# Kernel tuning notes

Hardware: AMD Instinct MI355X
Metric: run time of the kernel (lower is better)

Reference implementation:

```python
import jax, jax.numpy as jnp
import numpy as np

B, S, D = 2, 2048, 1024
H = 16
HD = D // H  # 64
SCALE = 1.0 / np.sqrt(HD).astype(np.float32)


def setup_inputs() -> dict:
    key = jax.random.key(0)
    ks = jax.random.split(key, 5)
    std = 0.02
    return {
        "x": jax.random.normal(ks[0], (B, S, D), dtype=jnp.float32),
        "W_qkv": jax.random.normal(ks[1], (D, 3 * D), dtype=jnp.float32) * std,
        "b_qkv": jnp.zeros((3 * D,), dtype=jnp.float32),
        "W_proj": jax.random.normal(ks[2], (D, D), dtype=jnp.float32) * std,
        "b_proj": jnp.zeros((D,), dtype=jnp.float32),
    }


def reference(x, W_qkv, b_qkv, W_proj, b_proj):
    bsz, seq_len, _ = x.shape
    qkv = x @ W_qkv + b_qkv  # [B,S,3D]
    qkv = qkv.reshape(bsz, seq_len, 3, H, HD)
    qkv = jnp.transpose(qkv, (2, 0, 3, 1, 4))  # [3,B,H,S,HD]
    q, k, v = qkv[0], qkv[1], qkv[2]
    scores = jnp.einsum("bhqd,bhkd->bhqk", q, k) * SCALE  # [B,H,S,S]
    causal = jnp.tril(jnp.ones((seq_len, seq_len), dtype=bool))
    scores = jnp.where(causal[None, None], scores, -jnp.inf)
    weights = jax.nn.softmax(scores, axis=-1)
    attn = jnp.einsum("bhqk,bhkd->bhqd", weights, v)  # [B,H,S,HD]
    attn = jnp.transpose(attn, (0, 2, 1, 3)).reshape(bsz, seq_len, H * HD)
    return attn @ W_proj + b_proj
```

## Files before the change

### kernel.cpp

```cpp
#include <hip/hip_runtime.h>
#include <stdint.h>

#define NB 2
#define NS 2048
#define ND 1024
#define NH 16
#define NHD 64
#define SCALE_QL2 0.1803368801111244f

typedef __attribute__((ext_vector_type(8))) short bf16x8;
typedef __attribute__((ext_vector_type(4))) float f32x4;
typedef __attribute__((ext_vector_type(16))) float f32x16;

__device__ __forceinline__ unsigned short f2bf(float f) {
  union { float f; unsigned u; } v; v.f = f;
  unsigned r = v.u + 0x7FFFu + ((v.u >> 16) & 1u);
  return (unsigned short)(r >> 16);
}

__device__ __forceinline__ float fexp2(float x) { return __builtin_amdgcn_exp2f(x); }

__device__ __forceinline__ unsigned cvtpk(float a, float b) {
  unsigned r;
  asm("v_cvt_pk_bf16_f32 %0, %1, %2" : "=v"(r) : "v"(a), "v"(b));
  return r;
}

__device__ __forceinline__ void plswap(unsigned& a, unsigned& b) {
  asm("v_permlane32_swap_b32 %0, %1" : "+v"(a), "+v"(b));
}

__device__ __forceinline__ void gload16(const void* g, void* l) {
  __builtin_amdgcn_global_load_lds(
      (const __attribute__((address_space(1))) unsigned int*)g,
      (__attribute__((address_space(3))) unsigned int*)l, 16, 0, 0);
}


__global__ void cvt_x(const float* __restrict__ in, unsigned short* __restrict__ out) {
  int i = blockIdx.x * 256 + threadIdx.x;
  const float4* p = (const float4*)in + (size_t)i * 2;
  float4 a = p[0], b = p[1];
  typedef __attribute__((ext_vector_type(8))) unsigned short u16x8;
  u16x8 o;
  o[0] = f2bf(a.x); o[1] = f2bf(a.y); o[2] = f2bf(a.z); o[3] = f2bf(a.w);
  o[4] = f2bf(b.x); o[5] = f2bf(b.y); o[6] = f2bf(b.z); o[7] = f2bf(b.w);
  *((u16x8*)out + i) = o;
}

__global__ void transpose_cvt(const float* __restrict__ W, unsigned short* __restrict__ WT,
                              int rows, int cols) {
  __shared__ float tile[32][33];
  int bc = blockIdx.x * 32;
  int br = blockIdx.y * 32;
  int tx = threadIdx.x & 31, ty = threadIdx.x >> 5;
#pragma unroll
  for (int i = 0; i < 4; ++i)
    tile[ty + i * 8][tx] = W[(size_t)(br + ty + i * 8) * cols + bc + tx];
  __syncthreads();
#pragma unroll
  for (int i = 0; i < 4; ++i)
    WT[(size_t)(bc + ty + i * 8) * rows + br + tx] = f2bf(tile[tx][ty + i * 8]);
}

template <int EPI>
__global__ __launch_bounds__(256, 2) void gemm_bt(
    const unsigned short* __restrict__ A, const unsigned short* __restrict__ Bt,
    const float* __restrict__ bias, int NT,
    unsigned short* __restrict__ Oq, unsigned short* __restrict__ Ok,
    unsigned short* __restrict__ Ov, float* __restrict__ Of) {
  __shared__ __align__(16) unsigned short lA[128 * 64];
  __shared__ __align__(16) unsigned short lB[128 * 64];

  int bid = blockIdx.x;
  int cpx = gridDim.x >> 3;
  int swz = (bid & 7) * cpx + (bid >> 3);
  int mt = swz / NT, nt = swz % NT;
  int m0 = mt * 128, n0 = nt * 128;

  int t = threadIdx.x, lane = t & 63, w = t >> 6;
  int wm = w >> 1, wn = w & 1;

  f32x4 acc[4][4] = {};

  const char* gA = (const char*)(A + (size_t)m0 * 1024);
  const char* gB = (const char*)(Bt + (size_t)n0 * 1024);

  for (int kt = 0; kt < 16; ++kt) {
    __syncthreads();
#pragma unroll
    for (int r = 0; r < 4; ++r) {
      int L = r * 4096 + w * 1024 + lane * 16;
      int row = L >> 7, cb = L & 127;
      int scb = cb ^ ((row & 7) << 4);
      gload16(gA + (size_t)row * 2048 + kt * 128 + scb, (char*)lA + (L - lane * 16));
      gload16(gB + (size_t)row * 2048 + kt * 128 + scb, (char*)lB + (L - lane * 16));
    }
    __syncthreads();
#pragma unroll
    for (int kk = 0; kk < 2; ++kk) {
      bf16x8 af[4], bg[4];
#pragma unroll
      for (int mi = 0; mi < 4; ++mi) {
        int row = wm * 64 + mi * 16 + (lane & 15);
        int byte = row * 128 + ((kk * 64 + (lane >> 4) * 16) ^ ((row & 7) << 4));
        af[mi] = *(const bf16x8*)((const char*)lA + byte);
      }
#pragma unroll
      for (int ni = 0; ni < 4; ++ni) {
        int row = wn * 64 + ni * 16 + (lane & 15);
        int byte = row * 128 + ((kk * 64 + (lane >> 4) * 16) ^ ((row & 7) << 4));
        bg[ni] = *(const bf16x8*)((const char*)lB + byte);
      }
#pragma unroll
      for (int mi = 0; mi < 4; ++mi)
#pragma unroll
        for (int ni = 0; ni < 4; ++ni)
          acc[mi][ni] = __builtin_amdgcn_mfma_f32_16x16x32_bf16(af[mi], bg[ni], acc[mi][ni], 0, 0, 0);
    }
  }

#pragma unroll
  for (int mi = 0; mi < 4; ++mi)
#pragma unroll
    for (int ni = 0; ni < 4; ++ni) {
      int col = n0 + wn * 64 + ni * 16 + (lane & 15);
      float bv = bias[col];
#pragma unroll
      for (int r = 0; r < 4; ++r) {
        int row = m0 + wm * 64 + mi * 16 + (lane >> 4) * 4 + r;
        float v = acc[mi][ni][r] + bv;
        if (EPI == 0) {
          int which = col >> 10, dd = col & 1023;
          int h = dd >> 6, hd = dd & 63;
          int b = row >> 11, s = row & 2047;
          size_t bh = (size_t)(b * 16 + h);
          if (which == 0)      Oq[(bh * 2048 + s) * 64 + hd] = f2bf(v * SCALE_QL2);
          else if (which == 1) Ok[(bh * 2048 + s) * 64 + hd] = f2bf(v);
          else                 Ov[(bh * 64 + hd) * 2048 + s] = f2bf(v);
        } else {
          Of[(size_t)row * 1024 + col] = v;
        }
      }
    }
}

__global__ __launch_bounds__(128, 2) void attn_fwd(
    const unsigned short* __restrict__ Qb, const unsigned short* __restrict__ Kb,
    const unsigned short* __restrict__ Vt, unsigned short* __restrict__ Ao) {
  __shared__ __align__(16) unsigned short lK[2][64 * 64];
  __shared__ __align__(16) unsigned short lV[2][64 * 64];

  int id = blockIdx.x;
  int qt = 31 - (id >> 5);
  int bh = id & 31;
  int t = threadIdx.x, lane = t & 63, w = t >> 6;
  int lo = lane & 31, hi = lane >> 5;
  int q0w = qt * 64 + w * 32;
  int swz = (lo & 7) << 4;

  const unsigned short* Qg = Qb + ((size_t)bh * 2048 + q0w + lo) * 64 + hi * 8;
  bf16x8 qf[4];
#pragma unroll
  for (int kk = 0; kk < 4; ++kk) qf[kk] = *(const bf16x8*)(Qg + kk * 16);

  f32x16 o0 = {}, o1 = {};
  float m = -1e30f, lsum = 0.f;

  const char* Kg = (const char*)(Kb + (size_t)bh * 2048 * 64);
  const char* Vg = (const char*)(Vt + (size_t)bh * 64 * 2048);

  int Lb = w * 4096 + lane * 16;
  auto STAGE = [&](int buf, int tile) {
    int s0 = tile * 64;
#pragma unroll
    for (int r = 0; r < 4; ++r) {
      int L = r * 1024 + Lb;
      int row = L >> 7, cb = L & 127;
      int scb = cb ^ ((row & 7) << 4);
      gload16(Kg + (size_t)(s0 + row) * 128 + scb, (char*)&lK[buf][0] + (L - lane * 16));
      gload16(Vg + (size_t)row * 4096 + (size_t)s0 * 2 + scb, (char*)&lV[buf][0] + (L - lane * 16));
    }
  };

  int ntiles = qt + 1;
  STAGE(0, 0);

  int cur = 0;
  for (int it = 0; it < ntiles; ++it) {
    if (it + 1 < ntiles) {
      STAGE(cur ^ 1, it + 1);
      asm volatile("s_waitcnt vmcnt(8)" ::: "memory");
    } else {
      asm volatile("s_waitcnt vmcnt(0)" ::: "memory");
    }
    asm volatile("s_barrier" ::: "memory");

    const char* bK = (const char*)&lK[cur][0];
    const char* bV = (const char*)&lV[cur][0];

    f32x16 sv0 = {}, sv1 = {};
    __builtin_amdgcn_s_setprio(1);
#pragma unroll
    for (int kk = 0; kk < 4; ++kk) {
      int dby = 32 * kk + 16 * hi;
      bf16x8 k0 = *(const bf16x8*)(bK + lo * 128 + (dby ^ swz));
      bf16x8 k1 = *(const bf16x8*)(bK + (32 + lo) * 128 + (dby ^ swz));
      sv0 = __builtin_amdgcn_mfma_f32_32x32x16_bf16(k0, qf[kk], sv0, 0, 0, 0);
      sv1 = __builtin_amdgcn_mfma_f32_32x32x16_bf16(k1, qf[kk], sv1, 0, 0, 0);
    }
    __builtin_amdgcn_s_setprio(0);

    if (it == ntiles - 1) {
      int qg = q0w + lo, s0 = it * 64;
#pragma unroll
      for (int r = 0; r < 16; ++r) {
        int kv = s0 + (r & 3) + 8 * (r >> 2) + 4 * hi;
        if (kv > qg) sv0[r] = -1e30f;
        if (kv + 32 > qg) sv1[r] = -1e30f;
      }
    }

    float rmax = -1e30f;
#pragma unroll
    for (int r = 0; r < 16; ++r) rmax = fmaxf(rmax, fmaxf(sv0[r], sv1[r]));
    rmax = fmaxf(rmax, __shfl_xor(rmax, 32));

    if (__any(rmax > m + 8.0f)) {
      float mn = fmaxf(m, rmax);
      float sf = fexp2(m - mn);
      m = mn; lsum *= sf;
#pragma unroll
      for (int r = 0; r < 16; ++r) {
        float s = __shfl(sf, (r & 3) + 8 * (r >> 2) + 4 * hi);
        o0[r] *= s; o1[r] *= s;
      }
    }

    float rsum = 0.f;
#pragma unroll
    for (int r = 0; r < 16; ++r) {
      sv0[r] = fexp2(sv0[r] - m); rsum += sv0[r];
      sv1[r] = fexp2(sv1[r] - m); rsum += sv1[r];
    }
    rsum += __shfl_xor(rsum, 32);
    lsum += rsum;

    bf16x8 pa[4];
#pragma unroll
    for (int h2 = 0; h2 < 2; ++h2) {
      const f32x16& P = h2 ? sv1 : sv0;
#pragma unroll
      for (int kp = 0; kp < 2; ++kp) {
        unsigned a0 = cvtpk(P[8 * kp + 0], P[8 * kp + 1]);
        unsigned a1 = cvtpk(P[8 * kp + 2], P[8 * kp + 3]);
        unsigned b0 = cvtpk(P[8 * kp + 4], P[8 * kp + 5]);
        unsigned b1 = cvtpk(P[8 * kp + 6], P[8 * kp + 7]);
        plswap(a0, b0); plswap(a1, b1);
        union { unsigned u[4]; bf16x8 v; } uu;
        uu.u[0] = a0; uu.u[1] = a1; uu.u[2] = b0; uu.u[3] = b1;
        pa[2 * h2 + kp] = uu.v;
      }
    }

    __builtin_amdgcn_s_setprio(1);
#pragma unroll
    for (int dh = 0; dh < 2; ++dh) {
      f32x16& oc = dh ? o1 : o0;
#pragma unroll
      for (int ks = 0; ks < 4; ++ks) {
        int kvby = 32 * ks + 16 * hi;
        bf16x8 vf = *(const bf16x8*)(bV + (32 * dh + lo) * 128 + (kvby ^ swz));
        oc = __builtin_amdgcn_mfma_f32_32x32x16_bf16(pa[ks], vf, oc, 0, 0, 0);
      }
    }
    __builtin_amdgcn_s_setprio(0);

    asm volatile("s_barrier" ::: "memory");
    cur ^= 1;
  }

  float rl = 1.0f / lsum;
  int b = bh >> 4, hh = bh & 15;
#pragma unroll
  for (int r = 0; r < 16; ++r) {
    int qrow = (r & 3) + 8 * (r >> 2) + 4 * hi;
    float s = __shfl(rl, qrow);
    size_t base = ((size_t)(b * 2048 + q0w + qrow)) * 1024 + hh * 64 + lo;
    Ao[base]      = f2bf(o0[r] * s);
    Ao[base + 32] = f2bf(o1[r] * s);
  }
}

extern "C" void kernel_launch(void* const* d_in, const int* in_sizes, int n_in,
                              void* d_out, int out_size, void* d_ws, size_t ws_size,
                              hipStream_t stream) {
  const float* x      = (const float*)d_in[0];
  const float* W_qkv  = (const float*)d_in[1];
  const float* b_qkv  = (const float*)d_in[2];
  const float* W_proj = (const float*)d_in[3];
  const float* b_proj = (const float*)d_in[4];
  float* out = (float*)d_out;

  char* ws = (char*)d_ws;
  const size_t MB = 1u << 20;
  unsigned short* xb     = (unsigned short*)(ws);
  unsigned short* WqkvT  = (unsigned short*)(ws + 8 * MB);
  unsigned short* WprojT = (unsigned short*)(ws + 14 * MB);
  unsigned short* Qb     = (unsigned short*)(ws + 16 * MB);
  unsigned short* Kb     = (unsigned short*)(ws + 24 * MB);
  unsigned short* Vt     = (unsigned short*)(ws + 32 * MB);
  unsigned short* attn   = xb;

  cvt_x<<<2048, 256, 0, stream>>>(x, xb);
  transpose_cvt<<<dim3(96, 32), 256, 0, stream>>>(W_qkv, WqkvT, 1024, 3072);
  transpose_cvt<<<dim3(32, 32), 256, 0, stream>>>(W_proj, WprojT, 1024, 1024);
  gemm_bt<0><<<768, 256, 0, stream>>>(xb, WqkvT, b_qkv, 24, Qb, Kb, Vt, nullptr);
  attn_fwd<<<1024, 128, 0, stream>>>(Qb, Kb, Vt, attn);
  gemm_bt<1><<<256, 256, 0, stream>>>(attn, WprojT, b_proj, 8, nullptr, nullptr, nullptr, out);
}
```

Baseline: 129.4 us.

## Split causal attention over KV chunks with a separate combine kernel

Causal attention is split along the key/value axis: each query tile is divided into chunks of up to 8 KV tiles, giving 2560 blocks of roughly equal work instead of 1024 blocks whose work varies 1 to 32 tiles. Each split writes unnormalized bf16 partial outputs plus row max and sum, and a new combine kernel merges them with log-sum-exp weighting. This targets load imbalance and the long tail from the largest query tiles. In exchange it adds an extra launch, partial-output traffic to workspace and a bf16 rounding of the partials. The path only runs when the workspace is large enough, otherwise the original kernel is used.

```diff
diff --git a/kernel.cpp b/kernel.cpp
--- a/kernel.cpp
+++ b/kernel.cpp
@@ -11,6 +11,7 @@
 typedef __attribute__((ext_vector_type(8))) short bf16x8;
 typedef __attribute__((ext_vector_type(4))) float f32x4;
 typedef __attribute__((ext_vector_type(16))) float f32x16;
+typedef __attribute__((ext_vector_type(8))) unsigned short u16x8;
 
 __device__ __forceinline__ unsigned short f2bf(float f) {
   union { float f; unsigned u; } v; v.f = f;
@@ -18,6 +19,11 @@
   return (unsigned short)(r >> 16);
 }
 
+__device__ __forceinline__ float bf2f(unsigned short u) {
+  union { unsigned u; float f; } v; v.u = ((unsigned)u) << 16;
+  return v.f;
+}
+
 __device__ __forceinline__ float fexp2(float x) { return __builtin_amdgcn_exp2f(x); }
 
 __device__ __forceinline__ unsigned cvtpk(float a, float b) {
@@ -41,7 +47,6 @@
   int i = blockIdx.x * 256 + threadIdx.x;
   const float4* p = (const float4*)in + (size_t)i * 2;
   float4 a = p[0], b = p[1];
-  typedef __attribute__((ext_vector_type(8))) unsigned short u16x8;
   u16x8 o;
   o[0] = f2bf(a.x); o[1] = f2bf(a.y); o[2] = f2bf(a.z); o[3] = f2bf(a.w);
   o[4] = f2bf(b.x); o[5] = f2bf(b.y); o[6] = f2bf(b.z); o[7] = f2bf(b.w);
@@ -145,19 +150,31 @@
     }
 }
 
-__global__ __launch_bounds__(128, 2) void attn_fwd(
+__global__ __launch_bounds__(128, 2) void attn_split(
     const unsigned short* __restrict__ Qb, const unsigned short* __restrict__ Kb,
-    const unsigned short* __restrict__ Vt, unsigned short* __restrict__ Ao) {
+    const unsigned short* __restrict__ Vt,
+    unsigned short* __restrict__ PO, float* __restrict__ PML) {
   __shared__ __align__(16) unsigned short lK[2][64 * 64];
   __shared__ __align__(16) unsigned short lV[2][64 * 64];
 
   int id = blockIdx.x;
-  int qt = 31 - (id >> 5);
   int bh = id & 31;
+  int slot = id >> 5;
+  int a, g;
+  if (slot < 8)       { a = 0; g = slot; }
+  else if (slot < 24) { a = 1; g = slot - 8; }
+  else if (slot < 48) { a = 2; g = slot - 24; }
+  else                { a = 3; g = slot - 48; }
+  int qg = (a == 0) ? g : (a == 1) ? (g >> 1) : (a == 2) ? ((g * 11) >> 5) : (g >> 2);
+  int qt = a * 8 + qg;
+  int c  = g - qg * (a + 1);
+  int t0 = c * 8;
+  int tend = min(t0 + 7, qt);
+
   int t = threadIdx.x, lane = t & 63, w = t >> 6;
   int lo = lane & 31, hi = lane >> 5;
   int q0w = qt * 64 + w * 32;
-  int swz = (lo & 7) << 4;
+  int swzb = (lo & 7) << 4;
 
   const unsigned short* Qg = Qb + ((size_t)bh * 2048 + q0w + lo) * 64 + hi * 8;
   bf16x8 qf[4];
@@ -183,12 +200,11 @@
     }
   };
 
-  int ntiles = qt + 1;
-  STAGE(0, 0);
+  STAGE(0, t0);
 
   int cur = 0;
-  for (int it = 0; it < ntiles; ++it) {
-    if (it + 1 < ntiles) {
+  for (int it = t0; it <= tend; ++it) {
+    if (it < tend) {
       STAGE(cur ^ 1, it + 1);
       asm volatile("s_waitcnt vmcnt(8)" ::: "memory");
     } else {
@@ -204,20 +220,20 @@
 #pragma unroll
     for (int kk = 0; kk < 4; ++kk) {
       int dby = 32 * kk + 16 * hi;
-      bf16x8 k0 = *(const bf16x8*)(bK + lo * 128 + (dby ^ swz));
-      bf16x8 k1 = *(const bf16x8*)(bK + (32 + lo) * 128 + (dby ^ swz));
+      bf16x8 k0 = *(const bf16x8*)(bK + lo * 128 + (dby ^ swzb));
+      bf16x8 k1 = *(const bf16x8*)(bK + (32 + lo) * 128 + (dby ^ swzb));
       sv0 = __builtin_amdgcn_mfma_f32_32x32x16_bf16(k0, qf[kk], sv0, 0, 0, 0);
       sv1 = __builtin_amdgcn_mfma_f32_32x32x16_bf16(k1, qf[kk], sv1, 0, 0, 0);
     }
     __builtin_amdgcn_s_setprio(0);
 
-    if (it == ntiles - 1) {
-      int qg = q0w + lo, s0 = it * 64;
+    if (it == qt) {
+      int qg2 = q0w + lo, s0 = it * 64;
 #pragma unroll
       for (int r = 0; r < 16; ++r) {
         int kv = s0 + (r & 3) + 8 * (r >> 2) + 4 * hi;
-        if (kv > qg) sv0[r] = -1e30f;
-        if (kv + 32 > qg) sv1[r] = -1e30f;
+        if (kv > qg2) sv0[r] = -1e30f;
+        if (kv + 32 > qg2) sv1[r] = -1e30f;
       }
     }
 
@@ -270,7 +286,200 @@
 #pragma unroll
       for (int ks = 0; ks < 4; ++ks) {
         int kvby = 32 * ks + 16 * hi;
-        bf16x8 vf = *(const bf16x8*)(bV + (32 * dh + lo) * 128 + (kvby ^ swz));
+        bf16x8 vf = *(const bf16x8*)(bV + (32 * dh + lo) * 128 + (kvby ^ swzb));
+        oc = __builtin_amdgcn_mfma_f32_32x32x16_bf16(pa[ks], vf, oc, 0, 0, 0);
+      }
+    }
+    __builtin_amdgcn_s_setprio(0);
+
+    asm volatile("s_barrier" ::: "memory");
+    cur ^= 1;
+  }
+
+  size_t pobase = (size_t)(bh * 80 + slot) * 64;
+#pragma unroll
+  for (int r = 0; r < 16; ++r) {
+    int crow = (r & 3) + 8 * (r >> 2) + 4 * hi;
+    size_t rowoff = (pobase + w * 32 + crow) * 64 + lo;
+    PO[rowoff]      = f2bf(o0[r]);
+    PO[rowoff + 32] = f2bf(o1[r]);
+  }
+  if (hi == 0) {
+    size_t mlbase = (size_t)(bh * 80 + slot) * 128 + w * 32 + lo;
+    PML[mlbase]      = m;
+    PML[mlbase + 64] = lsum;
+  }
+}
+
+__global__ void attn_combine(const unsigned short* __restrict__ PO,
+                             const float* __restrict__ PML,
+                             unsigned short* __restrict__ attn) {
+  int id = blockIdx.x * 256 + threadIdx.x;
+  int dg = id & 7;
+  int s  = (id >> 3) & 2047;
+  int bh = id >> 14;
+  int qt = s >> 6, a = qt >> 3;
+  int nc = a + 1;
+  int slot0 = (a + 1) * (qt - 4 * a);
+  int r64 = s & 63;
+  int pb = bh * 80 + slot0;
+
+  float mv[4], lv[4];
+#pragma unroll
+  for (int c = 0; c < 4; ++c) {
+    if (c < nc) {
+      mv[c] = PML[(size_t)(pb + c) * 128 + r64];
+      lv[c] = PML[(size_t)(pb + c) * 128 + 64 + r64];
+    } else { mv[c] = -1e30f; lv[c] = 0.f; }
+  }
+  float M = fmaxf(fmaxf(mv[0], mv[1]), fmaxf(mv[2], mv[3]));
+  float wv[4], L = 0.f;
+#pragma unroll
+  for (int c = 0; c < 4; ++c) { wv[c] = fexp2(mv[c] - M); L += wv[c] * lv[c]; }
+  float rcpL = 1.0f / L;
+
+  float acc[8] = {};
+#pragma unroll
+  for (int c = 0; c < 4; ++c) {
+    if (c < nc) {
+      bf16x8 p = *(const bf16x8*)(PO + ((size_t)(pb + c) * 64 + r64) * 64 + dg * 8);
+#pragma unroll
+      for (int j = 0; j < 8; ++j) acc[j] += wv[c] * bf2f((unsigned short)p[j]);
+    }
+  }
+  u16x8 o;
+#pragma unroll
+  for (int j = 0; j < 8; ++j) o[j] = f2bf(acc[j] * rcpL);
+  int b = bh >> 4, h = bh & 15;
+  *(u16x8*)(attn + ((size_t)(b * 2048 + s)) * 1024 + h * 64 + dg * 8) = o;
+}
+
+__global__ __launch_bounds__(128, 2) void attn_fwd(
+    const unsigned short* __restrict__ Qb, const unsigned short* __restrict__ Kb,
+    const unsigned short* __restrict__ Vt, unsigned short* __restrict__ Ao) {
+  __shared__ __align__(16) unsigned short lK[2][64 * 64];
+  __shared__ __align__(16) unsigned short lV[2][64 * 64];
+
+  int id = blockIdx.x;
+  int qt = 31 - (id >> 5);
+  int bh = id & 31;
+  int t = threadIdx.x, lane = t & 63, w = t >> 6;
+  int lo = lane & 31, hi = lane >> 5;
+  int q0w = qt * 64 + w * 32;
+  int swzb = (lo & 7) << 4;
+
+  const unsigned short* Qg = Qb + ((size_t)bh * 2048 + q0w + lo) * 64 + hi * 8;
+  bf16x8 qf[4];
+#pragma unroll
+  for (int kk = 0; kk < 4; ++kk) qf[kk] = *(const bf16x8*)(Qg + kk * 16);
+
+  f32x16 o0 = {}, o1 = {};
+  float m = -1e30f, lsum = 0.f;
+
+  const char* Kg = (const char*)(Kb + (size_t)bh * 2048 * 64);
+  const char* Vg = (const char*)(Vt + (size_t)bh * 64 * 2048);
+
+  int Lb = w * 4096 + lane * 16;
+  auto STAGE = [&](int buf, int tile) {
+    int s0 = tile * 64;
+#pragma unroll
+    for (int r = 0; r < 4; ++r) {
+      int L = r * 1024 + Lb;
+      int row = L >> 7, cb = L & 127;
+      int scb = cb ^ ((row & 7) << 4);
+      gload16(Kg + (size_t)(s0 + row) * 128 + scb, (char*)&lK[buf][0] + (L - lane * 16));
+      gload16(Vg + (size_t)row * 4096 + (size_t)s0 * 2 + scb, (char*)&lV[buf][0] + (L - lane * 16));
+    }
+  };
+
+  int ntiles = qt + 1;
+  STAGE(0, 0);
+
+  int cur = 0;
+  for (int it = 0; it < ntiles; ++it) {
+    if (it + 1 < ntiles) {
+      STAGE(cur ^ 1, it + 1);
+      asm volatile("s_waitcnt vmcnt(8)" ::: "memory");
+    } else {
+      asm volatile("s_waitcnt vmcnt(0)" ::: "memory");
+    }
+    asm volatile("s_barrier" ::: "memory");
+
+    const char* bK = (const char*)&lK[cur][0];
+    const char* bV = (const char*)&lV[cur][0];
+
+    f32x16 sv0 = {}, sv1 = {};
+    __builtin_amdgcn_s_setprio(1);
+#pragma unroll
+    for (int kk = 0; kk < 4; ++kk) {
+      int dby = 32 * kk + 16 * hi;
+      bf16x8 k0 = *(const bf16x8*)(bK + lo * 128 + (dby ^ swzb));
+      bf16x8 k1 = *(const bf16x8*)(bK + (32 + lo) * 128 + (dby ^ swzb));
+      sv0 = __builtin_amdgcn_mfma_f32_32x32x16_bf16(k0, qf[kk], sv0, 0, 0, 0);
+      sv1 = __builtin_amdgcn_mfma_f32_32x32x16_bf16(k1, qf[kk], sv1, 0, 0, 0);
+    }
+    __builtin_amdgcn_s_setprio(0);
+
+    if (it == ntiles - 1) {
+      int qg2 = q0w + lo, s0 = it * 64;
+#pragma unroll
+      for (int r = 0; r < 16; ++r) {
+        int kv = s0 + (r & 3) + 8 * (r >> 2) + 4 * hi;
+        if (kv > qg2) sv0[r] = -1e30f;
+        if (kv + 32 > qg2) sv1[r] = -1e30f;
+      }
+    }
+
+    float rmax = -1e30f;
+#pragma unroll
+    for (int r = 0; r < 16; ++r) rmax = fmaxf(rmax, fmaxf(sv0[r], sv1[r]));
+    rmax = fmaxf(rmax, __shfl_xor(rmax, 32));
+
+    if (__any(rmax > m + 8.0f)) {
+      float mn = fmaxf(m, rmax);
+      float sf = fexp2(m - mn);
+      m = mn; lsum *= sf;
+#pragma unroll
+      for (int r = 0; r < 16; ++r) {
+        float s = __shfl(sf, (r & 3) + 8 * (r >> 2) + 4 * hi);
+        o0[r] *= s; o1[r] *= s;
+      }
+    }
+
+    float rsum = 0.f;
+#pragma unroll
+    for (int r = 0; r < 16; ++r) {
+      sv0[r] = fexp2(sv0[r] - m); rsum += sv0[r];
+      sv1[r] = fexp2(sv1[r] - m); rsum += sv1[r];
+    }
+    rsum += __shfl_xor(rsum, 32);
+    lsum += rsum;
+
+    bf16x8 pa[4];
+#pragma unroll
+    for (int h2 = 0; h2 < 2; ++h2) {
+      const f32x16& P = h2 ? sv1 : sv0;
+#pragma unroll
+      for (int kp = 0; kp < 2; ++kp) {
+        unsigned a0 = cvtpk(P[8 * kp + 0], P[8 * kp + 1]);
+        unsigned a1 = cvtpk(P[8 * kp + 2], P[8 * kp + 3]);
+        unsigned b0 = cvtpk(P[8 * kp + 4], P[8 * kp + 5]);
+        unsigned b1 = cvtpk(P[8 * kp + 6], P[8 * kp + 7]);
+        plswap(a0, b0); plswap(a1, b1);
+        union { unsigned u[4]; bf16x8 v; } uu;
+        uu.u[0] = a0; uu.u[1] = a1; uu.u[2] = b0; uu.u[3] = b1;
+        pa[2 * h2 + kp] = uu.v;
+      }
+    }
+
+    __builtin_amdgcn_s_setprio(1);
+#pragma unroll
+    for (int dh = 0; dh < 2; ++dh) {
+      f32x16& oc = dh ? o1 : o0;
+#pragma unroll
+      for (int ks = 0; ks < 4; ++ks) {
+        int kvby = 32 * ks + 16 * hi;
+        bf16x8 vf = *(const bf16x8*)(bV + (32 * dh + lo) * 128 + (kvby ^ swzb));
         oc = __builtin_amdgcn_mfma_f32_32x32x16_bf16(pa[ks], vf, oc, 0, 0, 0);
       }
     }
@@ -310,12 +519,19 @@
   unsigned short* Qb     = (unsigned short*)(ws + 16 * MB);
   unsigned short* Kb     = (unsigned short*)(ws + 24 * MB);
   unsigned short* Vt     = (unsigned short*)(ws + 32 * MB);
+  unsigned short* PO     = (unsigned short*)(ws + 40 * MB);
+  float*          PML    = (float*)(ws + 60 * MB);
   unsigned short* attn   = xb;
 
   cvt_x<<<2048, 256, 0, stream>>>(x, xb);
   transpose_cvt<<<dim3(96, 32), 256, 0, stream>>>(W_qkv, WqkvT, 1024, 3072);
   transpose_cvt<<<dim3(32, 32), 256, 0, stream>>>(W_proj, WprojT, 1024, 1024);
   gemm_bt<0><<<768, 256, 0, stream>>>(xb, WqkvT, b_qkv, 24, Qb, Kb, Vt, nullptr);
-  attn_fwd<<<1024, 128, 0, stream>>>(Qb, Kb, Vt, attn);
+  if (ws_size >= 64225280ull) {
+    attn_split<<<2560, 128, 0, stream>>>(Qb, Kb, Vt, PO, PML);
+    attn_combine<<<2048, 256, 0, stream>>>(PO, PML, attn);
+  } else {
+    attn_fwd<<<1024, 128, 0, stream>>>(Qb, Kb, Vt, attn);
+  }
   gemm_bt<1><<<256, 256, 0, stream>>>(attn, WprojT, b_proj, 8, nullptr, nullptr, nullptr, out);
 }
```

Result: slower. 133.5 us (+3.1%).

## Split causal attention along KV into chunks with separate combine kernel

Applied to the files above, without the earlier changes.

Replaces the single-pass attention kernel with a split-KV version. Each block now covers 128 query rows and at most 8 KV tiles, giving 1280 more evenly sized blocks. Partial outputs plus row max and sum go to workspace, and a new combine kernel merges them with log-sum-exp weighting. This targets load imbalance from causal masking and low parallelism. The cost is an extra kernel launch, partial-result traffic, and bf16 rounding of unnormalized partials.

```diff
diff --git a/kernel.cpp b/kernel.cpp
--- a/kernel.cpp
+++ b/kernel.cpp
@@ -11,6 +11,7 @@
 typedef __attribute__((ext_vector_type(8))) short bf16x8;
 typedef __attribute__((ext_vector_type(4))) float f32x4;
 typedef __attribute__((ext_vector_type(16))) float f32x16;
+typedef __attribute__((ext_vector_type(8))) unsigned short u16x8;
 
 __device__ __forceinline__ unsigned short f2bf(float f) {
   union { float f; unsigned u; } v; v.f = f;
@@ -18,6 +19,11 @@
   return (unsigned short)(r >> 16);
 }
 
+__device__ __forceinline__ float bf2f(unsigned short u) {
+  union { unsigned u; float f; } v; v.u = ((unsigned)u) << 16;
+  return v.f;
+}
+
 __device__ __forceinline__ float fexp2(float x) { return __builtin_amdgcn_exp2f(x); }
 
 __device__ __forceinline__ unsigned cvtpk(float a, float b) {
@@ -41,7 +47,6 @@
   int i = blockIdx.x * 256 + threadIdx.x;
   const float4* p = (const float4*)in + (size_t)i * 2;
   float4 a = p[0], b = p[1];
-  typedef __attribute__((ext_vector_type(8))) unsigned short u16x8;
   u16x8 o;
   o[0] = f2bf(a.x); o[1] = f2bf(a.y); o[2] = f2bf(a.z); o[3] = f2bf(a.w);
   o[4] = f2bf(b.x); o[5] = f2bf(b.y); o[6] = f2bf(b.z); o[7] = f2bf(b.w);
@@ -145,19 +150,32 @@
     }
 }
 
-__global__ __launch_bounds__(128, 2) void attn_fwd(
+__global__ __launch_bounds__(256, 4) void attn_split(
     const unsigned short* __restrict__ Qb, const unsigned short* __restrict__ Kb,
-    const unsigned short* __restrict__ Vt, unsigned short* __restrict__ Ao) {
+    const unsigned short* __restrict__ Vt,
+    unsigned short* __restrict__ PO, float* __restrict__ PML) {
   __shared__ __align__(16) unsigned short lK[2][64 * 64];
   __shared__ __align__(16) unsigned short lV[2][64 * 64];
 
   int id = blockIdx.x;
-  int qt = 31 - (id >> 5);
   int bh = id & 31;
+  int slot = 39 - (id >> 5);
+  int a, g;
+  if (slot < 4)       { a = 0; g = slot; }
+  else if (slot < 12) { a = 1; g = slot - 4; }
+  else if (slot < 24) { a = 2; g = slot - 12; }
+  else                { a = 3; g = slot - 24; }
+  int Tg = (a == 0) ? g : (a == 1) ? (g >> 1) : (a == 2) ? ((g * 11) >> 5) : (g >> 2);
+  int T  = a * 4 + Tg;
+  int c  = g - Tg * (a + 1);
+  int t0 = c * 8;
+  int tend = min(t0 + 7, 2 * T + 1);
+
   int t = threadIdx.x, lane = t & 63, w = t >> 6;
   int lo = lane & 31, hi = lane >> 5;
-  int q0w = qt * 64 + w * 32;
-  int swz = (lo & 7) << 4;
+  int q0w = T * 128 + w * 32;
+  int itmaxw = 2 * T + (w >> 1);
+  int swzb = (lo & 7) << 4;
 
   const unsigned short* Qg = Qb + ((size_t)bh * 2048 + q0w + lo) * 64 + hi * 8;
   bf16x8 qf[4];
@@ -170,12 +188,12 @@
   const char* Kg = (const char*)(Kb + (size_t)bh * 2048 * 64);
   const char* Vg = (const char*)(Vt + (size_t)bh * 64 * 2048);
 
-  int Lb = w * 4096 + lane * 16;
+  int Lb = t * 16;
   auto STAGE = [&](int buf, int tile) {
     int s0 = tile * 64;
 #pragma unroll
-    for (int r = 0; r < 4; ++r) {
-      int L = r * 1024 + Lb;
+    for (int r = 0; r < 2; ++r) {
+      int L = r * 4096 + Lb;
       int row = L >> 7, cb = L & 127;
       int scb = cb ^ ((row & 7) << 4);
       gload16(Kg + (size_t)(s0 + row) * 128 + scb, (char*)&lK[buf][0] + (L - lane * 16));
@@ -183,113 +201,160 @@
     }
   };
 
-  int ntiles = qt + 1;
-  STAGE(0, 0);
+  STAGE(0, t0);
 
   int cur = 0;
-  for (int it = 0; it < ntiles; ++it) {
-    if (it + 1 < ntiles) {
+  for (int it = t0; it <= tend; ++it) {
+    if (it < tend) {
       STAGE(cur ^ 1, it + 1);
-      asm volatile("s_waitcnt vmcnt(8)" ::: "memory");
+      asm volatile("s_waitcnt vmcnt(4)" ::: "memory");
     } else {
       asm volatile("s_waitcnt vmcnt(0)" ::: "memory");
     }
     asm volatile("s_barrier" ::: "memory");
 
-    const char* bK = (const char*)&lK[cur][0];
-    const char* bV = (const char*)&lV[cur][0];
-
-    f32x16 sv0 = {}, sv1 = {};
-    __builtin_amdgcn_s_setprio(1);
-#pragma unroll
-    for (int kk = 0; kk < 4; ++kk) {
-      int dby = 32 * kk + 16 * hi;
-      bf16x8 k0 = *(const bf16x8*)(bK + lo * 128 + (dby ^ swz));
-      bf16x8 k1 = *(const bf16x8*)(bK + (32 + lo) * 128 + (dby ^ swz));
-      sv0 = __builtin_amdgcn_mfma_f32_32x32x16_bf16(k0, qf[kk], sv0, 0, 0, 0);
-      sv1 = __builtin_amdgcn_mfma_f32_32x32x16_bf16(k1, qf[kk], sv1, 0, 0, 0);
-    }
-    __builtin_amdgcn_s_setprio(0);
-
-    if (it == ntiles - 1) {
-      int qg = q0w + lo, s0 = it * 64;
+    if (it <= itmaxw) {
+      const char* bK = (const char*)&lK[cur][0];
+      const char* bV = (const char*)&lV[cur][0];
+
+      f32x16 sv0 = {}, sv1 = {};
+      __builtin_amdgcn_s_setprio(1);
+#pragma unroll
+      for (int kk = 0; kk < 4; ++kk) {
+        int dby = 32 * kk + 16 * hi;
+        bf16x8 k0 = *(const bf16x8*)(bK + lo * 128 + (dby ^ swzb));
+        bf16x8 k1 = *(const bf16x8*)(bK + (32 + lo) * 128 + (dby ^ swzb));
+        sv0 = __builtin_amdgcn_mfma_f32_32x32x16_bf16(k0, qf[kk], sv0, 0, 0, 0);
+        sv1 = __builtin_amdgcn_mfma_f32_32x32x16_bf16(k1, qf[kk], sv1, 0, 0, 0);
+      }
+      __builtin_amdgcn_s_setprio(0);
+
+      if (it == itmaxw) {
+        int qg2 = q0w + lo, s0 = it * 64;
+#pragma unroll
+        for (int r = 0; r < 16; ++r) {
+          int kv = s0 + (r & 3) + 8 * (r >> 2) + 4 * hi;
+          if (kv > qg2) sv0[r] = -1e30f;
+          if (kv + 32 > qg2) sv1[r] = -1e30f;
+        }
+      }
+
+      float rmax = -1e30f;
+#pragma unroll
+      for (int r = 0; r < 16; ++r) rmax = fmaxf(rmax, fmaxf(sv0[r], sv1[r]));
+      rmax = fmaxf(rmax, __shfl_xor(rmax, 32));
+
+      if (__any(rmax > m + 8.0f)) {
+        float mn = fmaxf(m, rmax);
+        float sf = fexp2(m - mn);
+        m = mn; lsum *= sf;
+#pragma unroll
+        for (int r = 0; r < 16; ++r) {
+          float s = __shfl(sf, (r & 3) + 8 * (r >> 2) + 4 * hi);
+          o0[r] *= s; o1[r] *= s;
+        }
+      }
+
+      float rsum = 0.f;
 #pragma unroll
       for (int r = 0; r < 16; ++r) {
-        int kv = s0 + (r & 3) + 8 * (r >> 2) + 4 * hi;
-        if (kv > qg) sv0[r] = -1e30f;
-        if (kv + 32 > qg) sv1[r] = -1e30f;
-      }
-    }
-
-    float rmax = -1e30f;
-#pragma unroll
-    for (int r = 0; r < 16; ++r) rmax = fmaxf(rmax, fmaxf(sv0[r], sv1[r]));
-    rmax = fmaxf(rmax, __shfl_xor(rmax, 32));
-
-    if (__any(rmax > m + 8.0f)) {
-      float mn = fmaxf(m, rmax);
-      float sf = fexp2(m - mn);
-      m = mn; lsum *= sf;
-#pragma unroll
-      for (int r = 0; r < 16; ++r) {
-        float s = __shfl(sf, (r & 3) + 8 * (r >> 2) + 4 * hi);
-        o0[r] *= s; o1[r] *= s;
-      }
-    }
-
-    float rsum = 0.f;
-#pragma unroll
-    for (int r = 0; r < 16; ++r) {
-      sv0[r] = fexp2(sv0[r] - m); rsum += sv0[r];
-      sv1[r] = fexp2(sv1[r] - m); rsum += sv1[r];
-    }
-    rsum += __shfl_xor(rsum, 32);
-    lsum += rsum;
-
-    bf16x8 pa[4];
-#pragma unroll
-    for (int h2 = 0; h2 < 2; ++h2) {
-      const f32x16& P = h2 ? sv1 : sv0;
-#pragma unroll
-      for (int kp = 0; kp < 2; ++kp) {
-        unsigned a0 = cvtpk(P[8 * kp + 0], P[8 * kp + 1]);
-        unsigned a1 = cvtpk(P[8 * kp + 2], P[8 * kp + 3]);
-        unsigned b0 = cvtpk(P[8 * kp + 4], P[8 * kp + 5]);
-        unsigned b1 = cvtpk(P[8 * kp + 6], P[8 * kp + 7]);
-        plswap(a0, b0); plswap(a1, b1);
-        union { unsigned u[4]; bf16x8 v; } uu;
-        uu.u[0] = a0; uu.u[1] = a1; uu.u[2] = b0; uu.u[3] = b1;
-        pa[2 * h2 + kp] = uu.v;
-      }
-    }
-
-    __builtin_amdgcn_s_setprio(1);
-#pragma unroll
-    for (int dh = 0; dh < 2; ++dh) {
-      f32x16& oc = dh ? o1 : o0;
-#pragma unroll
-      for (int ks = 0; ks < 4; ++ks) {
-        int kvby = 32 * ks + 16 * hi;
-        bf16x8 vf = *(const bf16x8*)(bV + (32 * dh + lo) * 128 + (kvby ^ swz));
-        oc = __builtin_amdgcn_mfma_f32_32x32x16_bf16(pa[ks], vf, oc, 0, 0, 0);
-      }
-    }
-    __builtin_amdgcn_s_setprio(0);
+        sv0[r] = fexp2(sv0[r] - m); rsum += sv0[r];
+        sv1[r] = fexp2(sv1[r] - m); rsum += sv1[r];
+      }
+      rsum += __shfl_xor(rsum, 32);
+      lsum += rsum;
+
+      bf16x8 pa[4];
+#pragma unroll
+      for (int h2 = 0; h2 < 2; ++h2) {
+        const f32x16& P = h2 ? sv1 : sv0;
+#pragma unroll
+        for (int kp = 0; kp < 2; ++kp) {
+          unsigned a0 = cvtpk(P[8 * kp + 0], P[8 * kp + 1]);
+          unsigned a1 = cvtpk(P[8 * kp + 2], P[8 * kp + 3]);
+          unsigned b0 = cvtpk(P[8 * kp + 4], P[8 * kp + 5]);
+          unsigned b1 = cvtpk(P[8 * kp + 6], P[8 * kp + 7]);
+          plswap(a0, b0); plswap(a1, b1);
+          union { unsigned u[4]; bf16x8 v; } uu;
+          uu.u[0] = a0; uu.u[1] = a1; uu.u[2] = b0; uu.u[3] = b1;
+          pa[2 * h2 + kp] = uu.v;
+        }
+      }
+
+      __builtin_amdgcn_s_setprio(1);
+#pragma unroll
+      for (int dh = 0; dh < 2; ++dh) {
+        f32x16& oc = dh ? o1 : o0;
+#pragma unroll
+        for (int ks = 0; ks < 4; ++ks) {
+          int kvby = 32 * ks + 16 * hi;
+          bf16x8 vf = *(const bf16x8*)(bV + (32 * dh + lo) * 128 + (kvby ^ swzb));
+          oc = __builtin_amdgcn_mfma_f32_32x32x16_bf16(pa[ks], vf, oc, 0, 0, 0);
+        }
+      }
+      __builtin_amdgcn_s_setprio(0);
+    }
 
     asm volatile("s_barrier" ::: "memory");
     cur ^= 1;
   }
 
-  float rl = 1.0f / lsum;
-  int b = bh >> 4, hh = bh & 15;
+  size_t pobase = (size_t)(bh * 40 + slot) * 128;
 #pragma unroll
   for (int r = 0; r < 16; ++r) {
-    int qrow = (r & 3) + 8 * (r >> 2) + 4 * hi;
-    float s = __shfl(rl, qrow);
-    size_t base = ((size_t)(b * 2048 + q0w + qrow)) * 1024 + hh * 64 + lo;
-    Ao[base]      = f2bf(o0[r] * s);
-    Ao[base + 32] = f2bf(o1[r] * s);
-  }
+    int crow = (r & 3) + 8 * (r >> 2) + 4 * hi;
+    size_t rowoff = (pobase + w * 32 + crow) * 64 + lo;
+    PO[rowoff]      = f2bf(o0[r]);
+    PO[rowoff + 32] = f2bf(o1[r]);
+  }
+  if (hi == 0) {
+    size_t mlbase = (size_t)(bh * 40 + slot) * 256 + w * 32 + lo;
+    PML[mlbase]       = m;
+    PML[mlbase + 128] = lsum;
+  }
+}
+
+__global__ void attn_combine(const unsigned short* __restrict__ PO,
+                             const float* __restrict__ PML,
+                             unsigned short* __restrict__ attn) {
+  int id = blockIdx.x * 256 + threadIdx.x;
+  int dg = id & 7;
+  int s  = (id >> 3) & 2047;
+  int bh = id >> 14;
+  int T = s >> 7, a = T >> 2;
+  int nc = a + 1;
+  int slot0 = (a + 1) * (T - 2 * a);
+  int r128 = s & 127;
+  int pb = bh * 40 + slot0;
+
+  float mv[4], lv[4];
+#pragma unroll
+  for (int c = 0; c < 4; ++c) {
+    if (c < nc) {
+      mv[c] = PML[(size_t)(pb + c) * 256 + r128];
+      lv[c] = PML[(size_t)(pb + c) * 256 + 128 + r128];
+    } else { mv[c] = -1e30f; lv[c] = 0.f; }
+  }
+  float M = fmaxf(fmaxf(mv[0], mv[1]), fmaxf(mv[2], mv[3]));
+  float wv[4], L = 0.f;
+#pragma unroll
+  for (int c = 0; c < 4; ++c) { wv[c] = fexp2(mv[c] - M); L += wv[c] * lv[c]; }
+  float rcpL = 1.0f / L;
+
+  float acc[8] = {};
+#pragma unroll
+  for (int c = 0; c < 4; ++c) {
+    if (c < nc) {
+      bf16x8 p = *(const bf16x8*)(PO + ((size_t)(pb + c) * 128 + r128) * 64 + dg * 8);
+#pragma unroll
+      for (int j = 0; j < 8; ++j) acc[j] += wv[c] * bf2f((unsigned short)p[j]);
+    }
+  }
+  u16x8 o;
+#pragma unroll
+  for (int j = 0; j < 8; ++j) o[j] = f2bf(acc[j] * rcpL);
+  int b = bh >> 4, h = bh & 15;
+  *(u16x8*)(attn + ((size_t)(b * 2048 + s)) * 1024 + h * 64 + dg * 8) = o;
 }
 
 extern "C" void kernel_launch(void* const* d_in, const int* in_sizes, int n_in,
@@ -310,12 +375,15 @@
   unsigned short* Qb     = (unsigned short*)(ws + 16 * MB);
   unsigned short* Kb     = (unsigned short*)(ws + 24 * MB);
   unsigned short* Vt     = (unsigned short*)(ws + 32 * MB);
+  unsigned short* PO     = (unsigned short*)(ws + 40 * MB);
+  float*          PML    = (float*)(ws + 60 * MB);
   unsigned short* attn   = xb;
 
   cvt_x<<<2048, 256, 0, stream>>>(x, xb);
   transpose_cvt<<<dim3(96, 32), 256, 0, stream>>>(W_qkv, WqkvT, 1024, 3072);
   transpose_cvt<<<dim3(32, 32), 256, 0, stream>>>(W_proj, WprojT, 1024, 1024);
   gemm_bt<0><<<768, 256, 0, stream>>>(xb, WqkvT, b_qkv, 24, Qb, Kb, Vt, nullptr);
-  attn_fwd<<<1024, 128, 0, stream>>>(Qb, Kb, Vt, attn);
+  attn_split<<<1280, 256, 0, stream>>>(Qb, Kb, Vt, PO, PML);
+  attn_combine<<<2048, 256, 0, stream>>>(PO, PML, attn);
   gemm_bt<1><<<256, 256, 0, stream>>>(attn, WprojT, b_proj, 8, nullptr, nullptr, nullptr, out);
 }
```

After: 124.6 us. 1.04x faster.
